# Kernel tuning notes

Hardware: AMD Instinct MI355X
Metric: run time of the kernel (lower is better)

## Reference

```python
import jax, jax.numpy as jnp
import numpy as np

D, H, DK, L, F, V = 512, 16, 32, 16, 1024, 32768
C1, C2, CORE, LG, MD, B = 512, 256, 256, 64, 64, 16
T_IN = C1 + C2 + CORE      # 1024
T_TF = CORE + LG + MD      # 384


def _ln(x, g, b, eps=1e-5):
    mu = x.mean(-1, keepdims=True)
    var = ((x - mu) ** 2).mean(-1, keepdims=True)
    return (x - mu) * jax.lax.rsqrt(var + eps) * g + b


def _heads(x):  # [B,T,D] -> [B,H,T,DK]
    b, t, _ = x.shape
    return x.reshape(b, t, H, DK).transpose(0, 2, 1, 3)


def _summarizer(ids, sem, pos, inw, inb, outw, outb, tok, lng, lnb):
    b, t = ids.shape
    x = sem[ids] + pos[:t][None]                      # [B,T,D]
    wq, wk, wv = jnp.split(inw, 3, axis=0)
    bq, bk, bv = jnp.split(inb, 3, axis=0)
    q = _heads(jnp.broadcast_to(tok, (b, tok.shape[1], D)) @ wq.T + bq)
    k = _heads(x @ wk.T + bk)
    v = _heads(x @ wv.T + bv)
    s = jnp.einsum('bhqd,bhkd->bhqk', q, k) / jnp.sqrt(jnp.float32(DK))
    a = jax.nn.softmax(s, axis=-1)
    o = jnp.einsum('bhqk,bhkd->bhqd', a, v).transpose(0, 2, 1, 3).reshape(b, -1, D)
    return _ln(o @ outw.T + outb, lng, lnb)


def _forward(emb_sem, emb_pos,
             lg_sem, lg_pos, lg_inw, lg_inb, lg_outw, lg_outb, lg_tok, lg_lng, lg_lnb,
             md_sem, md_pos, md_inw, md_inb, md_outw, md_outb, md_tok, md_lng, md_lnb,
             qkv_w, qkv_b, wo_w, wo_b, ln1_g, ln1_b, ln2_g, ln2_b,
             ff1_w, ff1_b, ff2_w, ff2_b, hd_lng, hd_lnb, hd_w, hd_b,
             input_ids, target_ids):
    lg_ids = input_ids[:, -(C1 + C2 + CORE):-(C2 + CORE)]
    md_ids = input_ids[:, -(C2 + CORE):-CORE]
    core_ids = input_ids[:, -CORE:]
    tgt = target_ids[:, -CORE:]

    lg_emb = _summarizer(lg_ids, lg_sem, lg_pos, lg_inw, lg_inb, lg_outw, lg_outb, lg_tok, lg_lng, lg_lnb)
    md_emb = _summarizer(md_ids, md_sem, md_pos, md_inw, md_inb, md_outw, md_outb, md_tok, md_lng, md_lnb)
    x_core = emb_sem[core_ids] + emb_pos[:CORE][None]
    x = jnp.concatenate([lg_emb, md_emb, x_core], axis=1)   # [B, 384, D]

    mask = jnp.tril(jnp.ones((T_TF, T_TF), dtype=bool))

    def step(x, p):
        qw, qb, ow, ob, g1, b1, g2, b2, f1w, f1b, f2w, f2b = p
        h = _ln(x, g1, b1)
        qkv = h @ qw.T + qb
        q, k, v = (_heads(t) for t in jnp.split(qkv, 3, axis=-1))
        s = jnp.einsum('bhqd,bhkd->bhqk', q, k) / jnp.sqrt(jnp.float32(DK))
        s = jnp.where(mask, s, -jnp.inf)
        a = jax.nn.softmax(s, axis=-1)
        o = jnp.einsum('bhqk,bhkd->bhqd', a, v).transpose(0, 2, 1, 3).reshape(x.shape)
        x = x + o @ ow.T + ob
        h2 = _ln(x, g2, b2)
        ff = jax.nn.gelu(h2 @ f1w.T + f1b, approximate=False) @ f2w.T + f2b
        return x + ff, None

    x, _ = jax.lax.scan(step, x, (qkv_w, qkv_b, wo_w, wo_b, ln1_g, ln1_b,
                                  ln2_g, ln2_b, ff1_w, ff1_b, ff2_w, ff2_b))
    logits = (_ln(x, hd_lng, hd_lnb) @ hd_w.T + hd_b)[:, -CORE:, :]
    return logits, tgt


def setup_inputs() -> dict:
    key = jax.random.key(0)
    ks = jax.random.split(key, 24)
    def rn(k, shape, s=0.02):
        return jax.random.normal(k, shape, jnp.float32) * s
    z, o = jnp.zeros, jnp.ones
    return {
        'input_ids': jax.random.randint(ks[0], (B, T_IN), 0, V),
        'target_ids': jax.random.randint(ks[1], (B, T_IN), 0, V),
        'emb_sem': rn(ks[2], (V, D)), 'emb_pos': rn(ks[3], (CORE, D)),
        'lg_sem': rn(ks[4], (V, D)), 'lg_pos': rn(ks[5], (C1, D)),
        'lg_inw': rn(ks[6], (3 * D, D)), 'lg_inb': z(3 * D),
        'lg_outw': rn(ks[7], (D, D)), 'lg_outb': z(D),
        'lg_tok': rn(ks[8], (1, LG, D), 1.0), 'lg_lng': o(D), 'lg_lnb': z(D),
        'md_sem': rn(ks[9], (V, D)), 'md_pos': rn(ks[10], (C2, D)),
        'md_inw': rn(ks[11], (3 * D, D)), 'md_inb': z(3 * D),
        'md_outw': rn(ks[12], (D, D)), 'md_outb': z(D),
        'md_tok': rn(ks[13], (1, MD, D), 1.0), 'md_lng': o(D), 'md_lnb': z(D),
        'qkv_w': rn(ks[14], (L, 3 * D, D)), 'qkv_b': z((L, 3 * D)),
        'wo_w': rn(ks[15], (L, D, D)), 'wo_b': z((L, D)),
        'ln1_g': o((L, D)), 'ln1_b': z((L, D)), 'ln2_g': o((L, D)), 'ln2_b': z((L, D)),
        'ff1_w': rn(ks[16], (L, F, D)), 'ff1_b': z((L, F)),
        'ff2_w': rn(ks[17], (L, D, F)), 'ff2_b': z((L, D)),
        'hd_lng': o(D), 'hd_lnb': z(D), 'hd_w': rn(ks[18], (V, D)), 'hd_b': z(V),
    }


def reference(input_ids, target_ids, emb_sem, emb_pos,
              lg_sem, lg_pos, lg_inw, lg_inb, lg_outw, lg_outb, lg_tok, lg_lng, lg_lnb,
              md_sem, md_pos, md_inw, md_inb, md_outw, md_outb, md_tok, md_lng, md_lnb,
              qkv_w, qkv_b, wo_w, wo_b, ln1_g, ln1_b, ln2_g, ln2_b,
              ff1_w, ff1_b, ff2_w, ff2_b, hd_lng, hd_lnb, hd_w, hd_b):
    return _forward(emb_sem, emb_pos,
                    lg_sem, lg_pos, lg_inw, lg_inb, lg_outw, lg_outb, lg_tok, lg_lng, lg_lnb,
                    md_sem, md_pos, md_inw, md_inb, md_outw, md_outb, md_tok, md_lng, md_lnb,
                    qkv_w, qkv_b, wo_w, wo_b, ln1_g, ln1_b, ln2_g, ln2_b,
                    ff1_w, ff1_b, ff2_w, ff2_b, hd_lng, hd_lnb, hd_w, hd_b,
                    input_ids, target_ids)
```

## Files before the change

### kernel.cpp

```cpp
#include <hip/hip_runtime.h>
#include <hip/hip_bf16.h>
#include <math.h>

#define D 512
#define NHEAD 16
#define DK 32
#define NLAYER 16
#define FF 1024
#define VOC 32768
#define TTF 384
#define NCORE 256
#define NB 16

typedef __attribute__((ext_vector_type(8))) short bfrag;
typedef __attribute__((ext_vector_type(4))) float f32x4;

typedef __attribute__((address_space(3))) void lds_void;
typedef const __attribute__((address_space(1))) void gbl_void;
__device__ __forceinline__ void gload16(const void* g, void* l) {
    __builtin_amdgcn_global_load_lds((gbl_void*)g, (lds_void*)l, 16, 0, 0);
}

__device__ __forceinline__ float gelu_f(float v) {
    return 0.5f * v * (1.0f + erff(v * 0.70710678118654752f));
}

__device__ __forceinline__ void bf8_to_f32(uint4 u, float* v) {
    const __hip_bfloat16* t = reinterpret_cast<const __hip_bfloat16*>(&u);
    #pragma unroll
    for (int e = 0; e < 8; e++) v[e] = __bfloat162float(t[e]);
}
__device__ __forceinline__ uint4 f32_to_bf8(const float* v) {
    uint4 u; __hip_bfloat16* t = reinterpret_cast<__hip_bfloat16*>(&u);
    #pragma unroll
    for (int e = 0; e < 8; e++) t[e] = __float2bfloat16(v[e]);
    return u;
}

__global__ __launch_bounds__(256) void cvtall_k(
    const float* s0, const float* s1, const float* s2, const float* s3,
    const float* s4, const float* s5, const float* s6, const float* s7,
    const float* s8, const float* s9, const float* s10,
    __hip_bfloat16* __restrict__ out)
{
    long long i = ((long long)blockIdx.x * 256 + threadIdx.x) * 8;
    if (i >= 52559872LL) return;
    const float* src; long long base; bool pad = false;
    if      (i < 12582912LL) { src = s0;  base = 0LL; }
    else if (i < 16777216LL) { src = s1;  base = 12582912LL; }
    else if (i < 25165824LL) { src = s2;  base = 16777216LL; }
    else if (i < 33554432LL) { src = s3;  base = 25165824LL; }
    else if (i < 50331648LL) { src = s4;  base = 33554432LL; }
    else if (i < 51118080LL) { src = s5;  base = 50331648LL; }
    else if (i < 51904512LL) { src = s6;  base = 51118080LL; }
    else if (i < 52166656LL) { src = s7;  base = 51904512LL; }
    else if (i < 52428800LL) { src = s8;  base = 52166656LL; }
    else if (i < 52494336LL) { src = s9;  base = 52428800LL; pad = true; }
    else                     { src = s10; base = 52494336LL; pad = true; }
    long long loc = i - base;
    float v[8] = {0.f,0.f,0.f,0.f,0.f,0.f,0.f,0.f};
    if (!pad || loc < 32768LL) {
        float4 a = *reinterpret_cast<const float4*>(src + loc);
        float4 b = *reinterpret_cast<const float4*>(src + loc + 4);
        v[0]=a.x; v[1]=a.y; v[2]=a.z; v[3]=a.w; v[4]=b.x; v[5]=b.y; v[6]=b.z; v[7]=b.w;
    }
    *reinterpret_cast<uint4*>(out + i) = f32_to_bf8(v);
}

__global__ __launch_bounds__(128) void embed_k(
    const int* __restrict__ ids, int id_stride, int id_off,
    const float* __restrict__ sem, const float* __restrict__ pos,
    __hip_bfloat16* __restrict__ out, int out_stride, int out_off)
{
    int t = blockIdx.x, b = blockIdx.y, tid = threadIdx.x;
    int id = ids[b * id_stride + id_off + t];
    const float4* s4 = reinterpret_cast<const float4*>(sem + (size_t)id * D);
    const float4* p4 = reinterpret_cast<const float4*>(pos + (size_t)t * D);
    size_t row = (size_t)(b * out_stride + out_off + t) * D;
    float4 a = s4[tid], p = p4[tid];
    __hip_bfloat16* o = out + row + tid * 4;
    o[0] = __float2bfloat16(a.x + p.x); o[1] = __float2bfloat16(a.y + p.y);
    o[2] = __float2bfloat16(a.z + p.z); o[3] = __float2bfloat16(a.w + p.w);
}

__global__ __launch_bounds__(256) void mgemm_k(
    const __hip_bfloat16* __restrict__ A, const __hip_bfloat16* __restrict__ W,
    const float* __restrict__ bias, void* __restrict__ C,
    int M, int N, int K, int flags, int order, int RT)
{
    __shared__ __align__(16) __hip_bfloat16 sA[2][8192];
    __shared__ __align__(16) __hip_bfloat16 sB[2][8192];
    int tid = threadIdx.x;
    int w = tid >> 6, lane = tid & 63;
    int wr = w >> 1, wc = w & 1;

    int nbx = gridDim.x, nby = gridDim.y;
    int nwg = nbx * nby;
    int bid0 = blockIdx.y * nbx + blockIdx.x;
    int bid = bid0;
    if (nwg >= 8) {
        int q = nwg >> 3, r = nwg & 7;
        int xcd = bid0 & 7, lb = bid0 >> 3;
        bid = (xcd < r ? xcd * (q + 1) : r * (q + 1) + (xcd - r) * q) + lb;
    }
    int bx, byg;
    if (order == 1) { bx = bid / nby; byg = bid - bx * nby; }
    else            { byg = bid / nbx; bx = bid - byg * nbx; }
    int col0 = bx * 128;

    int srow = lane >> 3;
    int scg  = (lane & 7) ^ srow;
    int cr = lane >> 4;
    int cc = lane & 15;

    auto stage = [&](int buf, int t, int k0) {
        int r0 = (byg * RT + t) * 128;
        #pragma unroll
        for (int r = 0; r < 4; r++) {
            int blk = r * 4 + w;
            const __hip_bfloat16* pa = A + (size_t)(r0 + blk * 8 + srow) * K + scg * 8 + k0;
            const __hip_bfloat16* pb = W + (size_t)(col0 + blk * 8 + srow) * K + scg * 8 + k0;
            gload16(pa, &sA[buf][blk * 512]);
            gload16(pb, &sB[buf][blk * 512]);
        }
    };

    int ksteps = K >> 6;
    int tsteps = RT * ksteps;

    stage(0, 0, 0);
    for (int t = 0; t < RT; t++) {
        int row0 = (byg * RT + t) * 128;

        f32x4 acc[4][4];
        #pragma unroll
        for (int m = 0; m < 4; m++)
            #pragma unroll
            for (int n = 0; n < 4; n++) acc[m][n] = (f32x4){0.f, 0.f, 0.f, 0.f};

        for (int kk = 0; kk < ksteps; kk++) {
            int s = t * ksteps + kk;
            int p = s & 1;
            if (s + 1 < tsteps) {
                int ns = s + 1;
                stage(p ^ 1, ns / ksteps, (ns % ksteps) << 6);
                asm volatile("s_waitcnt vmcnt(8)" ::: "memory");
            } else {
                asm volatile("s_waitcnt vmcnt(0)" ::: "memory");
            }
            __builtin_amdgcn_sched_barrier(0);
            __builtin_amdgcn_s_barrier();
            __builtin_amdgcn_sched_barrier(0);

            #pragma unroll
            for (int ks = 0; ks < 2; ks++) {
                bfrag af[4], bf[4];
                #pragma unroll
                for (int m = 0; m < 4; m++) {
                    int blk = wr * 8 + m * 2 + (cc >> 3);
                    int slot = (ks * 4 + cr) ^ (cc & 7);
                    af[m] = *reinterpret_cast<const bfrag*>(&sA[p][blk * 512 + (cc & 7) * 64 + slot * 8]);
                }
                #pragma unroll
                for (int n = 0; n < 4; n++) {
                    int blk = wc * 8 + n * 2 + (cc >> 3);
                    int slot = (ks * 4 + cr) ^ (cc & 7);
                    bf[n] = *reinterpret_cast<const bfrag*>(&sB[p][blk * 512 + (cc & 7) * 64 + slot * 8]);
                }
                #pragma unroll
                for (int m = 0; m < 4; m++)
                    #pragma unroll
                    for (int n = 0; n < 4; n++)
                        acc[m][n] = __builtin_amdgcn_mfma_f32_16x16x32_bf16(af[m], bf[n], acc[m][n], 0, 0, 0);
            }
            __builtin_amdgcn_sched_barrier(0);
            __builtin_amdgcn_s_barrier();
            __builtin_amdgcn_sched_barrier(0);
        }

        #pragma unroll
        for (int m = 0; m < 4; m++) {
            int rg = row0 + wr * 64 + m * 16 + cr * 4;
            #pragma unroll
            for (int n = 0; n < 4; n++) {
                int cg = col0 + wc * 64 + n * 16 + cc;
                float bs = bias[cg];
                #pragma unroll
                for (int j = 0; j < 4; j++) {
                    float v = acc[m][n][j] + bs;
                    size_t off = (size_t)(rg + j) * N + cg;
                    if (flags == 2)      ((__hip_bfloat16*)C)[off] = __float2bfloat16(gelu_f(v));
                    else if (flags == 3) ((__hip_bfloat16*)C)[off] = __float2bfloat16(v);
                    else                 ((float*)C)[off] = v;
                }
            }
        }
    }
}

template<int IB, int OB>
__global__ __launch_bounds__(256) void ln_k(
    const void* __restrict__ in, void* __restrict__ out,
    const float* __restrict__ g, const float* __restrict__ bt,
    int rpb, int in_stride, int in_off, int out_stride, int out_off)
{
    int r = blockIdx.x * 4 + (threadIdx.x >> 6);
    int b = r / rpb, t = r % rpb;
    size_t irow = (size_t)(b * in_stride + in_off + t) * D;
    size_t orow = (size_t)(b * out_stride + out_off + t) * D;
    int c0 = (threadIdx.x & 63) * 8;
    float v[8];
    if (IB) {
        bf8_to_f32(*reinterpret_cast<const uint4*>((const __hip_bfloat16*)in + irow + c0), v);
    } else {
        float4 a = *reinterpret_cast<const float4*>((const float*)in + irow + c0);
        float4 bq = *reinterpret_cast<const float4*>((const float*)in + irow + c0 + 4);
        v[0]=a.x; v[1]=a.y; v[2]=a.z; v[3]=a.w; v[4]=bq.x; v[5]=bq.y; v[6]=bq.z; v[7]=bq.w;
    }
    float s = 0.f;
    #pragma unroll
    for (int e = 0; e < 8; e++) s += v[e];
    #pragma unroll
    for (int off = 32; off; off >>= 1) s += __shfl_xor(s, off);
    float mu = s * (1.f / 512.f);
    float vs = 0.f;
    #pragma unroll
    for (int e = 0; e < 8; e++) { float d = v[e] - mu; vs += d * d; }
    #pragma unroll
    for (int off = 32; off; off >>= 1) vs += __shfl_xor(vs, off);
    float rstd = rsqrtf(vs * (1.f / 512.f) + 1e-5f);
    float y[8];
    #pragma unroll
    for (int e = 0; e < 8; e++) y[e] = (v[e] - mu) * rstd * g[c0 + e] + bt[c0 + e];
    if (OB) {
        *reinterpret_cast<uint4*>((__hip_bfloat16*)out + orow + c0) = f32_to_bf8(y);
    } else {
        *reinterpret_cast<float4*>((float*)out + orow + c0)     = make_float4(y[0], y[1], y[2], y[3]);
        *reinterpret_cast<float4*>((float*)out + orow + c0 + 4) = make_float4(y[4], y[5], y[6], y[7]);
    }
}

template<int WRITE_H>
__global__ __launch_bounds__(256) void res_ln_k(
    const __hip_bfloat16* __restrict__ delta, __hip_bfloat16* __restrict__ x,
    const float* __restrict__ g, const float* __restrict__ bt,
    __hip_bfloat16* __restrict__ h)
{
    int r = blockIdx.x * 4 + (threadIdx.x >> 6);
    int c0 = (threadIdx.x & 63) * 8;
    size_t row = (size_t)r * D + c0;
    float v[8], dv[8];
    bf8_to_f32(*reinterpret_cast<const uint4*>(x + row), v);
    bf8_to_f32(*reinterpret_cast<const uint4*>(delta + row), dv);
    #pragma unroll
    for (int e = 0; e < 8; e++) v[e] += dv[e];
    *reinterpret_cast<uint4*>(x + row) = f32_to_bf8(v);
    if (WRITE_H) {
        float s = 0.f;
        #pragma unroll
        for (int e = 0; e < 8; e++) s += v[e];
        #pragma unroll
        for (int off = 32; off; off >>= 1) s += __shfl_xor(s, off);
        float mu = s * (1.f / 512.f);
        float vs = 0.f;
        #pragma unroll
        for (int e = 0; e < 8; e++) { float d = v[e] - mu; vs += d * d; }
        #pragma unroll
        for (int off = 32; off; off >>= 1) vs += __shfl_xor(vs, off);
        float rstd = rsqrtf(vs * (1.f / 512.f) + 1e-5f);
        float y[8];
        #pragma unroll
        for (int e = 0; e < 8; e++) y[e] = (v[e] - mu) * rstd * g[c0 + e] + bt[c0 + e];
        *reinterpret_cast<uint4*>(h + row) = f32_to_bf8(y);
    }
}

__global__ __launch_bounds__(512) void fattn_k(
    const __hip_bfloat16* __restrict__ qkv, __hip_bfloat16* __restrict__ o)
{
    __shared__ __align__(16) __hip_bfloat16 Kl[24 * 512];
    __shared__ __align__(16) __hip_bfloat16 Vl[24 * 512];
    __shared__ __align__(16) __hip_bfloat16 Pl[8 * 512];
    int h = blockIdx.x, b = blockIdx.y, part = blockIdx.z;
    int tid = threadIdx.x, w = tid >> 6, l = tid & 63;
    const size_t base = (size_t)b * TTF * 1536 + h * DK;

    int niter = part ? 3 : 2;
    for (int it = 0; it < niter; it++) {
        int item = it * 512 + tid;
        int key = item >> 2, dg = item & 3;
        uint4 k4 = *reinterpret_cast<const uint4*>(qkv + base + (size_t)key * 1536 + 512 + dg * 8);
        *reinterpret_cast<uint4*>(&Kl[((key >> 4) * 64 + dg * 16 + (key & 15)) * 8]) = k4;
        uint4 v4 = *reinterpret_cast<const uint4*>(qkv + base + (size_t)key * 1536 + 1024 + dg * 8);
        const ushort* ve = reinterpret_cast<const ushort*>(&v4);
        #pragma unroll
        for (int e = 0; e < 8; e++) {
            int dk = dg * 8 + e;
            int f = (((key & 31) >> 3) << 4) | (dk & 15);
            int idx = (((key >> 5) << 1) + (dk >> 4)) * 512 + f * 8 + (key & 7);
            reinterpret_cast<ushort*>(Vl)[idx] = ve[e];
        }
    }
    __syncthreads();

    const float sc = 0.17677669529663687f;
    __hip_bfloat16* pw = Pl + w * 512;

    int niq = part ? 1 : 2;
    for (int iq = 0; iq < niq; iq++) {
        int qt = part ? (16 + w) : (iq == 0 ? w : 15 - w);
        int q0 = qt * 16;
        bfrag qf = *reinterpret_cast<const bfrag*>(qkv + base + (size_t)(q0 + (l & 15)) * 1536 + (l >> 4) * 8);
        f32x4 oa0 = (f32x4){0.f, 0.f, 0.f, 0.f};
        f32x4 oa1 = (f32x4){0.f, 0.f, 0.f, 0.f};
        float mrun[4], lrun[4];
        #pragma unroll
        for (int jj = 0; jj < 4; jj++) { mrun[jj] = -3.0e38f; lrun[jj] = 0.f; }
        int ksmax = (q0 + 15) >> 5;

        for (int ks = 0; ks <= ksmax; ks++) {
            bfrag kf0 = *reinterpret_cast<const bfrag*>(&Kl[(ks * 2 + 0) * 512 + l * 8]);
            bfrag kf1 = *reinterpret_cast<const bfrag*>(&Kl[(ks * 2 + 1) * 512 + l * 8]);
            f32x4 z = (f32x4){0.f, 0.f, 0.f, 0.f};
            __builtin_amdgcn_s_setprio(1);
            f32x4 s0 = __builtin_amdgcn_mfma_f32_16x16x32_bf16(qf, kf0, z, 0, 0, 0);
            f32x4 s1 = __builtin_amdgcn_mfma_f32_16x16x32_bf16(qf, kf1, z, 0, 0, 0);
            __builtin_amdgcn_s_setprio(0);
            if (ks == ksmax) {
                #pragma unroll
                for (int jj = 0; jj < 4; jj++) {
                    int q = q0 + ((l >> 4) << 2) + jj;
                    if (ks * 32 + (l & 15) > q)      s0[jj] = -3.0e38f;
                    if (ks * 32 + 16 + (l & 15) > q) s1[jj] = -3.0e38f;
                }
            }
            float p0[4], p1[4], ps[4];
            #pragma unroll
            for (int jj = 0; jj < 4; jj++) {
                float sm = fmaxf(s0[jj], s1[jj]);
                #pragma unroll
                for (int off = 1; off <= 8; off <<= 1) sm = fmaxf(sm, __shfl_xor(sm, off));
                float mnew = fmaxf(mrun[jj], sm);
                float f = __expf((mrun[jj] - mnew) * sc);
                mrun[jj] = mnew;
                lrun[jj] *= f;
                oa0[jj] *= f; oa1[jj] *= f;
                p0[jj] = __expf((s0[jj] - mnew) * sc);
                p1[jj] = __expf((s1[jj] - mnew) * sc);
                ps[jj] = p0[jj] + p1[jj];
            }
            #pragma unroll
            for (int jj = 0; jj < 4; jj++) {
                float t = ps[jj];
                #pragma unroll
                for (int off = 1; off <= 8; off <<= 1) t += __shfl_xor(t, off);
                lrun[jj] += t;
            }
            #pragma unroll
            for (int jj = 0; jj < 4; jj++) {
                int ql = ((l >> 4) << 2) + jj;
                int kl0 = l & 15, kl1 = 16 + (l & 15);
                pw[((kl0 >> 3) * 16 + ql) * 8 + (kl0 & 7)] = __float2bfloat16(p0[jj]);
                pw[((kl1 >> 3) * 16 + ql) * 8 + (kl1 & 7)] = __float2bfloat16(p1[jj]);
            }
            bfrag pf  = *reinterpret_cast<const bfrag*>(&pw[l * 8]);
            bfrag vf0 = *reinterpret_cast<const bfrag*>(&Vl[(ks * 2 + 0) * 512 + l * 8]);
            bfrag vf1 = *reinterpret_cast<const bfrag*>(&Vl[(ks * 2 + 1) * 512 + l * 8]);
            __builtin_amdgcn_s_setprio(1);
            oa0 = __builtin_amdgcn_mfma_f32_16x16x32_bf16(pf, vf0, oa0, 0, 0, 0);
            oa1 = __builtin_amdgcn_mfma_f32_16x16x32_bf16(pf, vf1, oa1, 0, 0, 0);
            __builtin_amdgcn_s_setprio(0);
        }
        #pragma unroll
        for (int jj = 0; jj < 4; jj++) {
            float inv = 1.0f / lrun[jj];
            int q = q0 + ((l >> 4) << 2) + jj;
            size_t orow = ((size_t)b * TTF + q) * D + h * DK;
            o[orow + (l & 15)]      = __float2bfloat16(oa0[jj] * inv);
            o[orow + 16 + (l & 15)] = __float2bfloat16(oa1[jj] * inv);
        }
    }
}

template<int TLEN>
__global__ __launch_bounds__(256) void sattn_k(
    const __hip_bfloat16* __restrict__ q, const __hip_bfloat16* __restrict__ kv,
    __hip_bfloat16* __restrict__ o)
{
    __shared__ __align__(16) __hip_bfloat16 Kl[(TLEN / 16) * 512];
    __shared__ __align__(16) __hip_bfloat16 Vl[(TLEN / 16) * 512];
    __shared__ __align__(16) __hip_bfloat16 Pl[4 * 512];
    int h = blockIdx.x, b = blockIdx.y;
    int tid = threadIdx.x, w = tid >> 6, l = tid & 63;

    for (int it = 0; it < TLEN / 64; it++) {
        int item = it * 256 + tid;
        int key = item >> 2, dg = item & 3;
        const __hip_bfloat16* kr = kv + (size_t)(b * TLEN + key) * 1024 + h * DK + dg * 8;
        uint4 k4 = *reinterpret_cast<const uint4*>(kr);
        *reinterpret_cast<uint4*>(&Kl[((key >> 4) * 64 + dg * 16 + (key & 15)) * 8]) = k4;
        uint4 v4 = *reinterpret_cast<const uint4*>(kr + 512);
        const ushort* ve = reinterpret_cast<const ushort*>(&v4);
        #pragma unroll
        for (int e = 0; e < 8; e++) {
            int dk = dg * 8 + e;
            int f = (((key & 31) >> 3) << 4) | (dk & 15);
            int idx = (((key >> 5) << 1) + (dk >> 4)) * 512 + f * 8 + (key & 7);
            reinterpret_cast<ushort*>(Vl)[idx] = ve[e];
        }
    }
    __syncthreads();

    const float sc = 0.17677669529663687f;
    __hip_bfloat16* pw = Pl + w * 512;
    int q0 = w * 16;
    bfrag qf = *reinterpret_cast<const bfrag*>(q + (size_t)(q0 + (l & 15)) * D + h * DK + (l >> 4) * 8);
    f32x4 oa0 = (f32x4){0.f, 0.f, 0.f, 0.f};
    f32x4 oa1 = (f32x4){0.f, 0.f, 0.f, 0.f};
    float mrun[4], lrun[4];
    #pragma unroll
    for (int jj = 0; jj < 4; jj++) { mrun[jj] = -3.0e38f; lrun[jj] = 0.f; }

    for (int ks = 0; ks < TLEN / 32; ks++) {
        bfrag kf0 = *reinterpret_cast<const bfrag*>(&Kl[(ks * 2 + 0) * 512 + l * 8]);
        bfrag kf1 = *reinterpret_cast<const bfrag*>(&Kl[(ks * 2 + 1) * 512 + l * 8]);
        f32x4 z = (f32x4){0.f, 0.f, 0.f, 0.f};
        __builtin_amdgcn_s_setprio(1);
        f32x4 s0 = __builtin_amdgcn_mfma_f32_16x16x32_bf16(qf, kf0, z, 0, 0, 0);
        f32x4 s1 = __builtin_amdgcn_mfma_f32_16x16x32_bf16(qf, kf1, z, 0, 0, 0);
        __builtin_amdgcn_s_setprio(0);
        float p0[4], p1[4], ps[4];
        #pragma unroll
        for (int jj = 0; jj < 4; jj++) {
            float sm = fmaxf(s0[jj], s1[jj]);
            #pragma unroll
            for (int off = 1; off <= 8; off <<= 1) sm = fmaxf(sm, __shfl_xor(sm, off));
            float mnew = fmaxf(mrun[jj], sm);
            float f = __expf((mrun[jj] - mnew) * sc);
            mrun[jj] = mnew;
            lrun[jj] *= f;
            oa0[jj] *= f; oa1[jj] *= f;
            p0[jj] = __expf((s0[jj] - mnew) * sc);
            p1[jj] = __expf((s1[jj] - mnew) * sc);
            ps[jj] = p0[jj] + p1[jj];
        }
        #pragma unroll
        for (int jj = 0; jj < 4; jj++) {
            float t = ps[jj];
            #pragma unroll
            for (int off = 1; off <= 8; off <<= 1) t += __shfl_xor(t, off);
            lrun[jj] += t;
        }
        #pragma unroll
        for (int jj = 0; jj < 4; jj++) {
            int ql = ((l >> 4) << 2) + jj;
            int kl0 = l & 15, kl1 = 16 + (l & 15);
            pw[((kl0 >> 3) * 16 + ql) * 8 + (kl0 & 7)] = __float2bfloat16(p0[jj]);
            pw[((kl1 >> 3) * 16 + ql) * 8 + (kl1 & 7)] = __float2bfloat16(p1[jj]);
        }
        bfrag pf  = *reinterpret_cast<const bfrag*>(&pw[l * 8]);
        bfrag vf0 = *reinterpret_cast<const bfrag*>(&Vl[(ks * 2 + 0) * 512 + l * 8]);
        bfrag vf1 = *reinterpret_cast<const bfrag*>(&Vl[(ks * 2 + 1) * 512 + l * 8]);
        __builtin_amdgcn_s_setprio(1);
        oa0 = __builtin_amdgcn_mfma_f32_16x16x32_bf16(pf, vf0, oa0, 0, 0, 0);
        oa1 = __builtin_amdgcn_mfma_f32_16x16x32_bf16(pf, vf1, oa1, 0, 0, 0);
        __builtin_amdgcn_s_setprio(0);
    }
    #pragma unroll
    for (int jj = 0; jj < 4; jj++) {
        float inv = 1.0f / lrun[jj];
        int qi = q0 + ((l >> 4) << 2) + jj;
        size_t orow = ((size_t)b * 64 + qi) * D + h * DK;
        o[orow + (l & 15)]      = __float2bfloat16(oa0[jj] * inv);
        o[orow + 16 + (l & 15)] = __float2bfloat16(oa1[jj] * inv);
    }
}

__global__ __launch_bounds__(256) void tgt_k(const int* __restrict__ tids, float* __restrict__ out)
{
    int i = blockIdx.x * 256 + threadIdx.x;
    int b = i >> 8, c = i & 255;
    out[i] = (float)tids[b * 1024 + 768 + c];
}

extern "C" void kernel_launch(void* const* d_in, const int* in_sizes, int n_in,
                              void* d_out, int out_size, void* d_ws, size_t ws_size,
                              hipStream_t stream) {
    (void)in_sizes; (void)n_in; (void)out_size; (void)ws_size;
    const int*   input_ids  = (const int*)  d_in[0];
    const int*   target_ids = (const int*)  d_in[1];
    const float* emb_sem    = (const float*)d_in[2];
    const float* emb_pos    = (const float*)d_in[3];
    const float* lg_sem     = (const float*)d_in[4];
    const float* lg_pos     = (const float*)d_in[5];
    const float* lg_inw     = (const float*)d_in[6];
    const float* lg_inb     = (const float*)d_in[7];
    const float* lg_outw    = (const float*)d_in[8];
    const float* lg_outb    = (const float*)d_in[9];
    const float* lg_tok     = (const float*)d_in[10];
    const float* lg_lng     = (const float*)d_in[11];
    const float* lg_lnb     = (const float*)d_in[12];
    const float* md_sem     = (const float*)d_in[13];
    const float* md_pos     = (const float*)d_in[14];
    const float* md_inw     = (const float*)d_in[15];
    const float* md_inb     = (const float*)d_in[16];
    const float* md_outw    = (const float*)d_in[17];
    const float* md_outb    = (const float*)d_in[18];
    const float* md_tok     = (const float*)d_in[19];
    const float* md_lng     = (const float*)d_in[20];
    const float* md_lnb     = (const float*)d_in[21];
    const float* qkv_w      = (const float*)d_in[22];
    const float* qkv_b      = (const float*)d_in[23];
    const float* wo_w       = (const float*)d_in[24];
    const float* wo_b       = (const float*)d_in[25];
    const float* ln1_g      = (const float*)d_in[26];
    const float* ln1_b      = (const float*)d_in[27];
    const float* ln2_g      = (const float*)d_in[28];
    const float* ln2_b      = (const float*)d_in[29];
    const float* ff1_w      = (const float*)d_in[30];
    const float* ff1_b      = (const float*)d_in[31];
    const float* ff2_w      = (const float*)d_in[32];
    const float* ff2_b      = (const float*)d_in[33];
    const float* hd_lng     = (const float*)d_in[34];
    const float* hd_lnb     = (const float*)d_in[35];
    const float* hd_w       = (const float*)d_in[36];
    const float* hd_b       = (const float*)d_in[37];

    __hip_bfloat16* x_bf   = (__hip_bfloat16*)d_ws;
    __hip_bfloat16* h_bf   = x_bf   + 3145728;
    __hip_bfloat16* d_bf   = h_bf   + 3145728;
    __hip_bfloat16* a_bf   = d_bf   + 3145728;
    __hip_bfloat16* qkv_bf = a_bf   + 6291456;
    __hip_bfloat16* sumo_bf= qkv_bf + 9437184;
    __hip_bfloat16* w_qkv  = sumo_bf+ 524288;
    __hip_bfloat16* w_wo   = w_qkv  + 12582912;
    __hip_bfloat16* w_ff1  = w_wo   + 4194304;
    __hip_bfloat16* w_ff2  = w_ff1  + 8388608;
    __hip_bfloat16* w_hd   = w_ff2  + 8388608;
    __hip_bfloat16* w_lgin = w_hd   + 16777216;
    __hip_bfloat16* w_mdin = w_lgin + 786432;
    __hip_bfloat16* w_lgout= w_mdin + 786432;
    __hip_bfloat16* w_mdout= w_lgout+ 262144;
    __hip_bfloat16* tok_lg = w_mdout+ 262144;
    __hip_bfloat16* tok_md = tok_lg + 65536;
    __hip_bfloat16* q_bf   = tok_md + 65536;
    float* so2 = (float*)(q_bf + 65536);

    cvtall_k<<<25664, 256, 0, stream>>>(qkv_w, wo_w, ff1_w, ff2_w, hd_w,
                                        lg_inw, md_inw, lg_outw, md_outw,
                                        lg_tok, md_tok, w_qkv);

    embed_k<<<dim3(512, NB), 128, 0, stream>>>(input_ids, 1024, 0, lg_sem, lg_pos, a_bf, 512, 0);
    mgemm_k<<<dim3(8, 64), 256, 0, stream>>>(a_bf, w_lgin + 512 * 512, lg_inb + 512, qkv_bf, 8192, 1024, 512, 3, 0, 1);
    mgemm_k<<<dim3(4, 1), 256, 0, stream>>>(tok_lg, w_lgin, lg_inb, q_bf, 128, 512, 512, 3, 0, 1);
    sattn_k<512><<<dim3(NHEAD, NB), 256, 0, stream>>>(q_bf, qkv_bf, sumo_bf);
    mgemm_k<<<dim3(4, 8), 256, 0, stream>>>(sumo_bf, w_lgout, lg_outb, so2, 1024, 512, 512, 0, 0, 1);
    ln_k<0, 1><<<256, 256, 0, stream>>>(so2, x_bf, lg_lng, lg_lnb, 64, 64, 0, TTF, 0);

    embed_k<<<dim3(256, NB), 128, 0, stream>>>(input_ids, 1024, 512, md_sem, md_pos, a_bf, 256, 0);
    mgemm_k<<<dim3(8, 32), 256, 0, stream>>>(a_bf, w_mdin + 512 * 512, md_inb + 512, qkv_bf, 4096, 1024, 512, 3, 0, 1);
    mgemm_k<<<dim3(4, 1), 256, 0, stream>>>(tok_md, w_mdin, md_inb, q_bf, 128, 512, 512, 3, 0, 1);
    sattn_k<256><<<dim3(NHEAD, NB), 256, 0, stream>>>(q_bf, qkv_bf, sumo_bf);
    mgemm_k<<<dim3(4, 8), 256, 0, stream>>>(sumo_bf, w_mdout, md_outb, so2, 1024, 512, 512, 0, 0, 1);
    ln_k<0, 1><<<256, 256, 0, stream>>>(so2, x_bf, md_lng, md_lnb, 64, 64, 0, TTF, 64);

    embed_k<<<dim3(256, NB), 128, 0, stream>>>(input_ids, 1024, 768, emb_sem, emb_pos, x_bf, TTF, 128);

    ln_k<1, 1><<<1536, 256, 0, stream>>>(x_bf, h_bf, ln1_g, ln1_b, TTF, TTF, 0, TTF, 0);
    for (int l = 0; l < NLAYER; l++) {
        mgemm_k<<<dim3(12, 48), 256, 0, stream>>>(h_bf, w_qkv + (size_t)l * 1536 * 512, qkv_b + l * 1536, qkv_bf, 6144, 1536, 512, 3, 0, 1);
        fattn_k<<<dim3(NHEAD, NB, 2), 512, 0, stream>>>(qkv_bf, a_bf);
        mgemm_k<<<dim3(4, 48), 256, 0, stream>>>(a_bf, w_wo + (size_t)l * 512 * 512, wo_b + l * D, d_bf, 6144, 512, 512, 3, 0, 1);
        res_ln_k<1><<<1536, 256, 0, stream>>>(d_bf, x_bf, ln2_g + l * D, ln2_b + l * D, h_bf);
        mgemm_k<<<dim3(8, 48), 256, 0, stream>>>(h_bf, w_ff1 + (size_t)l * 1024 * 512, ff1_b + l * FF, a_bf, 6144, 1024, 512, 2, 0, 1);
        mgemm_k<<<dim3(4, 48), 256, 0, stream>>>(a_bf, w_ff2 + (size_t)l * 512 * 1024, ff2_b + l * D, d_bf, 6144, 512, 1024, 3, 0, 1);
        if (l < NLAYER - 1) {
            res_ln_k<1><<<1536, 256, 0, stream>>>(d_bf, x_bf, ln1_g + (size_t)(l + 1) * D, ln1_b + (size_t)(l + 1) * D, h_bf);
        } else {
            res_ln_k<0><<<1536, 256, 0, stream>>>(d_bf, x_bf, hd_lng, hd_lnb, h_bf);
        }
    }

    ln_k<1, 1><<<1024, 256, 0, stream>>>(x_bf, h_bf, hd_lng, hd_lnb, NCORE, TTF, 128, NCORE, 0);
    float* logits = (float*)d_out;
    mgemm_k<<<dim3(256, 4), 256, 0, stream>>>(h_bf, w_hd, hd_b, logits, 4096, VOC, 512, 0, 1, 8);
    tgt_k<<<16, 256, 0, stream>>>(target_ids, logits + (size_t)NB * NCORE * VOC);
}
```

Before: 2.679 ms.

## Fuse residual add into GEMM epilogue, merge embedding kernels, relax tile-boundary wait

The Wo and FF2 GEMMs now add their output in place into the bf16 residual stream, using a read-modify-write epilogue. A plain LayerNorm kernel then replaces the separate residual+LN kernel, which removes the delta buffer round trip. The three embedding launches are merged into one kernel that writes the md embeddings to a separate offset, so fewer launches are needed. The GEMM also skips the vmcnt wait on the first k-step of each new row tile (vmcnt(63)), which may race on pipelined loads when RT>1. The RMW epilogue adds a scattered global read per output element.

```diff
diff --git a/kernel.cpp b/kernel.cpp
--- a/kernel.cpp
+++ b/kernel.cpp
@@ -67,18 +67,25 @@
     *reinterpret_cast<uint4*>(out + i) = f32_to_bf8(v);
 }
 
-__global__ __launch_bounds__(128) void embed_k(
-    const int* __restrict__ ids, int id_stride, int id_off,
-    const float* __restrict__ sem, const float* __restrict__ pos,
-    __hip_bfloat16* __restrict__ out, int out_stride, int out_off)
-{
-    int t = blockIdx.x, b = blockIdx.y, tid = threadIdx.x;
-    int id = ids[b * id_stride + id_off + t];
-    const float4* s4 = reinterpret_cast<const float4*>(sem + (size_t)id * D);
-    const float4* p4 = reinterpret_cast<const float4*>(pos + (size_t)t * D);
-    size_t row = (size_t)(b * out_stride + out_off + t) * D;
-    float4 a = s4[tid], p = p4[tid];
-    __hip_bfloat16* o = out + row + tid * 4;
+__global__ __launch_bounds__(128) void embed_all_k(
+    const int* __restrict__ ids,
+    const float* __restrict__ lg_sem, const float* __restrict__ lg_pos,
+    const float* __restrict__ md_sem, const float* __restrict__ md_pos,
+    const float* __restrict__ em_sem, const float* __restrict__ em_pos,
+    __hip_bfloat16* __restrict__ lg_dst, __hip_bfloat16* __restrict__ md_dst,
+    __hip_bfloat16* __restrict__ x)
+{
+    int bx = blockIdx.x, b = blockIdx.y, tid = threadIdx.x;
+    const float *sem, *pos;
+    __hip_bfloat16* outp;
+    int t, idoff;
+    if (bx < 512)      { t = bx;       sem = lg_sem; pos = lg_pos; idoff = 0;   outp = lg_dst + (size_t)(b * 512 + t) * D; }
+    else if (bx < 768) { t = bx - 512; sem = md_sem; pos = md_pos; idoff = 512; outp = md_dst + (size_t)(b * 256 + t) * D; }
+    else               { t = bx - 768; sem = em_sem; pos = em_pos; idoff = 768; outp = x + (size_t)(b * TTF + 128 + t) * D; }
+    int id = ids[b * 1024 + idoff + t];
+    float4 a = reinterpret_cast<const float4*>(sem + (size_t)id * D)[tid];
+    float4 p = reinterpret_cast<const float4*>(pos + (size_t)t * D)[tid];
+    __hip_bfloat16* o = outp + tid * 4;
     o[0] = __float2bfloat16(a.x + p.x); o[1] = __float2bfloat16(a.y + p.y);
     o[2] = __float2bfloat16(a.z + p.z); o[3] = __float2bfloat16(a.w + p.w);
 }
@@ -144,7 +151,11 @@
             if (s + 1 < tsteps) {
                 int ns = s + 1;
                 stage(p ^ 1, ns / ksteps, (ns % ksteps) << 6);
-                asm volatile("s_waitcnt vmcnt(8)" ::: "memory");
+                if (kk == 0 && t > 0) {
+                    asm volatile("s_waitcnt vmcnt(63)" ::: "memory");
+                } else {
+                    asm volatile("s_waitcnt vmcnt(8)" ::: "memory");
+                }
             } else {
                 asm volatile("s_waitcnt vmcnt(0)" ::: "memory");
             }
@@ -191,6 +202,10 @@
                     size_t off = (size_t)(rg + j) * N + cg;
                     if (flags == 2)      ((__hip_bfloat16*)C)[off] = __float2bfloat16(gelu_f(v));
                     else if (flags == 3) ((__hip_bfloat16*)C)[off] = __float2bfloat16(v);
+                    else if (flags == 4) {
+                        __hip_bfloat16* cp = (__hip_bfloat16*)C + off;
+                        *cp = __float2bfloat16(v + __bfloat162float(*cp));
+                    }
                     else                 ((float*)C)[off] = v;
                 }
             }
@@ -237,41 +252,6 @@
     } else {
         *reinterpret_cast<float4*>((float*)out + orow + c0)     = make_float4(y[0], y[1], y[2], y[3]);
         *reinterpret_cast<float4*>((float*)out + orow + c0 + 4) = make_float4(y[4], y[5], y[6], y[7]);
-    }
-}
-
-template<int WRITE_H>
-__global__ __launch_bounds__(256) void res_ln_k(
-    const __hip_bfloat16* __restrict__ delta, __hip_bfloat16* __restrict__ x,
-    const float* __restrict__ g, const float* __restrict__ bt,
-    __hip_bfloat16* __restrict__ h)
-{
-    int r = blockIdx.x * 4 + (threadIdx.x >> 6);
-    int c0 = (threadIdx.x & 63) * 8;
-    size_t row = (size_t)r * D + c0;
-    float v[8], dv[8];
-    bf8_to_f32(*reinterpret_cast<const uint4*>(x + row), v);
-    bf8_to_f32(*reinterpret_cast<const uint4*>(delta + row), dv);
-    #pragma unroll
-    for (int e = 0; e < 8; e++) v[e] += dv[e];
-    *reinterpret_cast<uint4*>(x + row) = f32_to_bf8(v);
-    if (WRITE_H) {
-        float s = 0.f;
-        #pragma unroll
-        for (int e = 0; e < 8; e++) s += v[e];
-        #pragma unroll
-        for (int off = 32; off; off >>= 1) s += __shfl_xor(s, off);
-        float mu = s * (1.f / 512.f);
-        float vs = 0.f;
-        #pragma unroll
-        for (int e = 0; e < 8; e++) { float d = v[e] - mu; vs += d * d; }
-        #pragma unroll
-        for (int off = 32; off; off >>= 1) vs += __shfl_xor(vs, off);
-        float rstd = rsqrtf(vs * (1.f / 512.f) + 1e-5f);
-        float y[8];
-        #pragma unroll
-        for (int e = 0; e < 8; e++) y[e] = (v[e] - mu) * rstd * g[c0 + e] + bt[c0 + e];
-        *reinterpret_cast<uint4*>(h + row) = f32_to_bf8(y);
     }
 }
 
@@ -550,34 +530,32 @@
                                         lg_inw, md_inw, lg_outw, md_outw,
                                         lg_tok, md_tok, w_qkv);
 
-    embed_k<<<dim3(512, NB), 128, 0, stream>>>(input_ids, 1024, 0, lg_sem, lg_pos, a_bf, 512, 0);
+    embed_all_k<<<dim3(1024, NB), 128, 0, stream>>>(input_ids,
+        lg_sem, lg_pos, md_sem, md_pos, emb_sem, emb_pos,
+        a_bf, a_bf + 4194304, x_bf);
+
     mgemm_k<<<dim3(8, 64), 256, 0, stream>>>(a_bf, w_lgin + 512 * 512, lg_inb + 512, qkv_bf, 8192, 1024, 512, 3, 0, 1);
     mgemm_k<<<dim3(4, 1), 256, 0, stream>>>(tok_lg, w_lgin, lg_inb, q_bf, 128, 512, 512, 3, 0, 1);
     sattn_k<512><<<dim3(NHEAD, NB), 256, 0, stream>>>(q_bf, qkv_bf, sumo_bf);
     mgemm_k<<<dim3(4, 8), 256, 0, stream>>>(sumo_bf, w_lgout, lg_outb, so2, 1024, 512, 512, 0, 0, 1);
     ln_k<0, 1><<<256, 256, 0, stream>>>(so2, x_bf, lg_lng, lg_lnb, 64, 64, 0, TTF, 0);
 
-    embed_k<<<dim3(256, NB), 128, 0, stream>>>(input_ids, 1024, 512, md_sem, md_pos, a_bf, 256, 0);
-    mgemm_k<<<dim3(8, 32), 256, 0, stream>>>(a_bf, w_mdin + 512 * 512, md_inb + 512, qkv_bf, 4096, 1024, 512, 3, 0, 1);
+    mgemm_k<<<dim3(8, 32), 256, 0, stream>>>(a_bf + 4194304, w_mdin + 512 * 512, md_inb + 512, qkv_bf, 4096, 1024, 512, 3, 0, 1);
     mgemm_k<<<dim3(4, 1), 256, 0, stream>>>(tok_md, w_mdin, md_inb, q_bf, 128, 512, 512, 3, 0, 1);
     sattn_k<256><<<dim3(NHEAD, NB), 256, 0, stream>>>(q_bf, qkv_bf, sumo_bf);
     mgemm_k<<<dim3(4, 8), 256, 0, stream>>>(sumo_bf, w_mdout, md_outb, so2, 1024, 512, 512, 0, 0, 1);
     ln_k<0, 1><<<256, 256, 0, stream>>>(so2, x_bf, md_lng, md_lnb, 64, 64, 0, TTF, 64);
 
-    embed_k<<<dim3(256, NB), 128, 0, stream>>>(input_ids, 1024, 768, emb_sem, emb_pos, x_bf, TTF, 128);
-
     ln_k<1, 1><<<1536, 256, 0, stream>>>(x_bf, h_bf, ln1_g, ln1_b, TTF, TTF, 0, TTF, 0);
     for (int l = 0; l < NLAYER; l++) {
         mgemm_k<<<dim3(12, 48), 256, 0, stream>>>(h_bf, w_qkv + (size_t)l * 1536 * 512, qkv_b + l * 1536, qkv_bf, 6144, 1536, 512, 3, 0, 1);
         fattn_k<<<dim3(NHEAD, NB, 2), 512, 0, stream>>>(qkv_bf, a_bf);
-        mgemm_k<<<dim3(4, 48), 256, 0, stream>>>(a_bf, w_wo + (size_t)l * 512 * 512, wo_b + l * D, d_bf, 6144, 512, 512, 3, 0, 1);
-        res_ln_k<1><<<1536, 256, 0, stream>>>(d_bf, x_bf, ln2_g + l * D, ln2_b + l * D, h_bf);
+        mgemm_k<<<dim3(4, 48), 256, 0, stream>>>(a_bf, w_wo + (size_t)l * 512 * 512, wo_b + l * D, x_bf, 6144, 512, 512, 4, 0, 1);
+        ln_k<1, 1><<<1536, 256, 0, stream>>>(x_bf, h_bf, ln2_g + l * D, ln2_b + l * D, TTF, TTF, 0, TTF, 0);
         mgemm_k<<<dim3(8, 48), 256, 0, stream>>>(h_bf, w_ff1 + (size_t)l * 1024 * 512, ff1_b + l * FF, a_bf, 6144, 1024, 512, 2, 0, 1);
-        mgemm_k<<<dim3(4, 48), 256, 0, stream>>>(a_bf, w_ff2 + (size_t)l * 512 * 1024, ff2_b + l * D, d_bf, 6144, 512, 1024, 3, 0, 1);
+        mgemm_k<<<dim3(4, 48), 256, 0, stream>>>(a_bf, w_ff2 + (size_t)l * 512 * 1024, ff2_b + l * D, x_bf, 6144, 512, 1024, 4, 0, 1);
         if (l < NLAYER - 1) {
-            res_ln_k<1><<<1536, 256, 0, stream>>>(d_bf, x_bf, ln1_g + (size_t)(l + 1) * D, ln1_b + (size_t)(l + 1) * D, h_bf);
-        } else {
-            res_ln_k<0><<<1536, 256, 0, stream>>>(d_bf, x_bf, hd_lng, hd_lnb, h_bf);
+            ln_k<1, 1><<<1536, 256, 0, stream>>>(x_bf, h_bf, ln1_g + (size_t)(l + 1) * D, ln1_b + (size_t)(l + 1) * D, TTF, TTF, 0, TTF, 0);
         }
     }
 
```

Measured after the change: 2.943 ms. 9.9% more time.
